# Kernel tuning notes

Measured on AMD Instinct MI355X. Metric: run time of the kernel, lower is better.

## Reference

```python
import jax, jax.numpy as jnp
import numpy as np

N = 100000   # nodes
E = 200000   # edges
L = 3        # GNN layers
D = 300      # node feature dim
H = 150      # per-direction message dim


def setup_inputs() -> dict:
    key = jax.random.key(0)
    ks = jax.random.split(key, 8)
    s = 0.05
    return {
        "x": jax.random.normal(ks[0], (N, D), jnp.float32),
        "edge_index": jax.random.randint(ks[1], (2, E), 0, N, dtype=jnp.int32),
        "Wr": jax.random.normal(ks[2], (L, 2 * D, H), jnp.float32) * s,
        "br": jax.random.normal(ks[3], (L, H), jnp.float32) * s,
        "Wc": jax.random.normal(ks[4], (L, 2 * D, H), jnp.float32) * s,
        "bc": jax.random.normal(ks[5], (L, H), jnp.float32) * s,
        "Wa": jax.random.normal(ks[6], (D, D), jnp.float32) * s,
        "ba": jax.random.normal(ks[7], (D,), jnp.float32) * s,
    }


def _gelu(z):
    return jax.nn.gelu(z, approximate=False)  # torch GELU is exact erf


def _msg_aggr(v, src, dst, W, b):
    # message at each edge: GELU(Linear(cat(x_i, x_j))), x_i = target, x_j = source
    m = _gelu(jnp.concatenate([v[dst], v[src]], axis=-1) @ W + b)  # [E, H]
    # sum-aggregate messages at target nodes
    return jax.ops.segment_sum(m, dst, num_segments=N)  # [N, H]


def reference(x, edge_index, Wr, br, Wc, bc, Wa, ba):
    src, dst = edge_index[0], edge_index[1]

    def step(v, p):
        Wr_l, br_l, Wc_l, bc_l = p
        r = _msg_aggr(v, src, dst, Wr_l, br_l)        # r2c: original direction
        c = _msg_aggr(v, dst, src, Wc_l, bc_l)        # c2r: flipped edge_index
        v = v + _gelu(jnp.concatenate([r, c], axis=-1) @ Wa + ba)
        return v, None

    out, _ = jax.lax.scan(step, x, (Wr, br, Wc, bc))
    return out
```

## Files before the change

### kernel.cpp

```cpp
#include <hip/hip_runtime.h>
#include <hip/hip_bf16.h>
#include <math.h>

#define NND 100000
#define EE  200000
#define LL  3
#define DD  300
#define HH  150

#define MPAD 100096
#define KP   320
#define NPJ  640
#define NUP  384
#define NTK  (KP / 32)

#define NB   49
#define SCN  (NB * 2048)

#define BSTRIDE 132

#define P_BR 0
#define P_BC 152
#define P_AR 304
#define P_AC 456
#define RC_R 0
#define RC_C 160

typedef __attribute__((ext_vector_type(8))) short bf16x8;
typedef __attribute__((ext_vector_type(4))) short bf16x4;
typedef __attribute__((ext_vector_type(4))) float f32x4;

__device__ __forceinline__ float gelu_exact(float z) {
    return 0.5f * z * (1.0f + erff(z * 0.7071067811865475f));
}
__device__ __forceinline__ unsigned short f2bf(float f) {
    union { float fv; unsigned u; } v; v.fv = f;
    unsigned r = v.u + 0x7fff + ((v.u >> 16) & 1);
    return (unsigned short)(r >> 16);
}
__device__ __forceinline__ float bf2f(unsigned short b) {
    union { unsigned u; float fv; } v; v.u = ((unsigned)b) << 16;
    return v.fv;
}

__global__ __launch_bounds__(256) void pack_w(
    const float* __restrict__ Wr, const float* __restrict__ Wc,
    const float* __restrict__ Wa,
    unsigned short* __restrict__ Bt, unsigned short* __restrict__ Wat)
{
    int i = blockIdx.x * 256 + threadIdx.x;
    const int btTotal = LL * NPJ * KP;
    if (i < btTotal) {
        int l = i / (NPJ * KP);
        int rem = i % (NPJ * KP);
        int n = rem / KP;
        int k = rem % KP;
        float v = 0.f;
        if (k < DD) {
            const float* W = nullptr; int krow = k, j = -1;
            if (n >= P_BR && n < P_BR + 150)      { W = Wr; krow = 300 + k; j = n - P_BR; }
            else if (n >= P_BC && n < P_BC + 150) { W = Wc; krow = 300 + k; j = n - P_BC; }
            else if (n >= P_AR && n < P_AR + 150) { W = Wr; krow = k;       j = n - P_AR; }
            else if (n >= P_AC && n < P_AC + 150) { W = Wc; krow = k;       j = n - P_AC; }
            if (j >= 0)
                v = W[(size_t)l * 600 * 150 + (size_t)krow * 150 + j];
        }
        Bt[i] = f2bf(v);
    } else {
        int i2 = i - btTotal;
        if (i2 < NUP * KP) {
            int n = i2 / KP, k = i2 % KP;
            int kk = -1;
            if (k < 150)                 kk = k;
            else if (k >= 160 && k < 310) kk = k - 10;
            float v = (n < DD && kk >= 0) ? Wa[(size_t)kk * DD + n] : 0.f;
            Wat[i2] = f2bf(v);
        }
    }
}

__global__ __launch_bounds__(256) void init_vbf(
    const float* __restrict__ x, unsigned short* __restrict__ vbf)
{
    int idx = blockIdx.x * 256 + threadIdx.x;
    int row = idx / (KP / 8);
    int gk  = (idx % (KP / 8)) * 8;
    if (row >= MPAD) return;
    unsigned short tmp[8];
    if (row < NND && gk < DD) {
        if (gk + 8 <= DD) {
            const float4* p = (const float4*)(x + (size_t)row * DD + gk);
            float4 f0 = p[0], f1 = p[1];
            tmp[0] = f2bf(f0.x); tmp[1] = f2bf(f0.y);
            tmp[2] = f2bf(f0.z); tmp[3] = f2bf(f0.w);
            tmp[4] = f2bf(f1.x); tmp[5] = f2bf(f1.y);
            tmp[6] = f2bf(f1.z); tmp[7] = f2bf(f1.w);
        } else {
            #pragma unroll
            for (int j = 0; j < 8; ++j)
                tmp[j] = (gk + j < DD) ? f2bf(x[(size_t)row * DD + gk + j]) : 0;
        }
    } else {
        #pragma unroll
        for (int j = 0; j < 8; ++j) tmp[j] = 0;
    }
    *((bf16x8*)&vbf[(size_t)row * KP + gk]) = *((bf16x8*)tmp);
}

__global__ __launch_bounds__(256) void hist_deg(
    const int* __restrict__ src, const int* __restrict__ dst,
    int* __restrict__ deg)
{
    int e = blockIdx.x * 256 + threadIdx.x;
    if (e >= EE) return;
    atomicAdd(&deg[dst[e]], 1);
    atomicAdd(&deg[SCN + src[e]], 1);
}

__global__ __launch_bounds__(256) void scanA(
    const int* __restrict__ deg, int* __restrict__ off, int* __restrict__ bsum)
{
    __shared__ int ls[256];
    const int t = threadIdx.x, row = blockIdx.y;
    const int base = blockIdx.x * 2048 + t * 8;
    const int* dg = deg + (size_t)row * SCN + base;
    int v[8];
    #pragma unroll
    for (int j = 0; j < 8; ++j) v[j] = dg[j];
    int tot = 0;
    #pragma unroll
    for (int j = 0; j < 8; ++j) tot += v[j];
    ls[t] = tot;
    __syncthreads();
    #pragma unroll
    for (int d = 1; d < 256; d <<= 1) {
        int tv = (t >= d) ? ls[t - d] : 0;
        __syncthreads();
        ls[t] += tv;
        __syncthreads();
    }
    int run = ls[t] - tot;
    int* op = off + (size_t)row * SCN + base;
    #pragma unroll
    for (int j = 0; j < 8; ++j) { op[j] = run; run += v[j]; }
    if (t == 255) bsum[row * 64 + blockIdx.x] = ls[255];
}

__global__ __launch_bounds__(256) void scanB(int* __restrict__ bsum)
{
    if (threadIdx.x < 2) {
        int row = threadIdx.x, c = 0;
        for (int i = 0; i < NB; ++i) {
            int tv = bsum[row * 64 + i];
            bsum[row * 64 + i] = c;
            c += tv;
        }
    }
}

__global__ __launch_bounds__(256) void scanC(
    int* __restrict__ off, const int* __restrict__ bsum, int* __restrict__ cur)
{
    const int t = threadIdx.x, row = blockIdx.y;
    const int base = blockIdx.x * 2048 + t * 8;
    const int add = bsum[row * 64 + blockIdx.x];
    int* op = off + (size_t)row * SCN + base;
    int* cp = cur + (size_t)row * SCN + base;
    #pragma unroll
    for (int j = 0; j < 8; ++j) {
        int v = op[j] + add;
        op[j] = v;
        cp[j] = v;
    }
}

__global__ __launch_bounds__(256) void fill_adj(
    const int* __restrict__ src, const int* __restrict__ dst,
    int* __restrict__ cur, int* __restrict__ adj)
{
    int e = blockIdx.x * 256 + threadIdx.x;
    if (e >= EE) return;
    int s = src[e], d = dst[e];
    int pd = atomicAdd(&cur[d], 1);
    adj[pd] = s;
    int ps = atomicAdd(&cur[SCN + s], 1);
    adj[EE + ps] = d;
}

__global__ __launch_bounds__(256) void aggregate(
    const int* __restrict__ off, const int* __restrict__ adj,
    const unsigned short* __restrict__ P,
    const float* __restrict__ br, const float* __restrict__ bc,
    unsigned short* __restrict__ RC)
{
    const int n    = blockIdx.x * 4 + (threadIdx.x >> 6);
    const int dir  = blockIdx.y;
    const int lane = threadIdx.x & 63;
    const int c    = lane * 4;

    if (lane < 10)
        RC[(size_t)n * KP + (dir ? 310 : 150) + lane] = 0;
    if (c >= 152) return;

    const int* offp = off + (size_t)dir * SCN;
    const int* adjp = adj + (size_t)dir * EE;
    const float* bias = dir ? bc : br;
    const unsigned short* own = P + (size_t)n * NPJ + (dir ? P_AC : P_AR);
    const int poff = dir ? P_BC : P_BR;

    const bool g0 = (c + 0) < 150, g1 = (c + 1) < 150;
    const bool g2 = (c + 2) < 150, g3 = (c + 3) < 150;

    bf16x4 ow = *((const bf16x4*)&own[c]);
    float o0 = bf2f((unsigned short)ow[0]) + (g0 ? bias[c + 0] : 0.f);
    float o1 = bf2f((unsigned short)ow[1]) + (g1 ? bias[c + 1] : 0.f);
    float o2 = bf2f((unsigned short)ow[2]) + (g2 ? bias[c + 2] : 0.f);
    float o3 = bf2f((unsigned short)ow[3]) + (g3 ? bias[c + 3] : 0.f);

    float s0 = 0.f, s1 = 0.f, s2 = 0.f, s3 = 0.f;
    int beg = offp[n], end = offp[n + 1];
    if (beg < end) {
        int a = adjp[beg];
        for (int i = beg; i < end; ++i) {
            int anext = (i + 1 < end) ? adjp[i + 1] : 0;
            const unsigned short* pp = P + (size_t)a * NPJ + poff;
            bf16x4 pv = *((const bf16x4*)&pp[c]);
            s0 += gelu_exact(o0 + bf2f((unsigned short)pv[0]));
            s1 += gelu_exact(o1 + bf2f((unsigned short)pv[1]));
            s2 += gelu_exact(o2 + bf2f((unsigned short)pv[2]));
            s3 += gelu_exact(o3 + bf2f((unsigned short)pv[3]));
            a = anext;
        }
    }
    unsigned short* outrow = RC + (size_t)n * KP + (dir ? RC_C : RC_R);
    if (c + 4 <= 150) {
        bf16x4 o;
        o[0] = (short)f2bf(s0); o[1] = (short)f2bf(s1);
        o[2] = (short)f2bf(s2); o[3] = (short)f2bf(s3);
        *((bf16x4*)&outrow[c]) = o;
    } else {
        if (g0) outrow[c + 0] = f2bf(s0);
        if (g1) outrow[c + 1] = f2bf(s1);
    }
}

#define GLOAD16(gp, lp) __builtin_amdgcn_global_load_lds( \
    (const __attribute__((address_space(1))) unsigned int*)(gp), \
    (__attribute__((address_space(3))) unsigned int*)(lp), 16, 0, 0)

template<int MODE>
__global__ __launch_bounds__(256) void gemm_breg(
    const unsigned short* __restrict__ Ab,
    const unsigned short* __restrict__ Bt,
    unsigned short* __restrict__ P,
    float* __restrict__ outv, unsigned short* __restrict__ vbf,
    const float* __restrict__ bias, int last)
{
    __shared__ char smem[64 * BSTRIDE * 4];
    unsigned short* Alds = (unsigned short*)smem;
    float* bounce = (float*)smem;

    const int tid  = threadIdx.x;
    const int lane = tid & 63;
    const int wid  = tid >> 6;

    const int gx   = gridDim.x;
    const int nwg  = gx * gridDim.y;
    const int flat = blockIdx.y * gx + blockIdx.x;
    const int q = nwg >> 3, r = nwg & 7;
    const int xcd = flat & 7, off = flat >> 3;
    const int lid = (xcd < r ? xcd * (q + 1) : r * (q + 1) + (xcd - r) * q) + off;
    const int brow = (lid / gx) * 64;
    const int bcol = (lid % gx) * 128;

    const int wn = wid * 32;

    f32x4 acc[4][2];
    #pragma unroll
    for (int i = 0; i < 4; ++i)
        #pragma unroll
        for (int j = 0; j < 2; ++j)
            #pragma unroll
            for (int rr = 0; rr < 4; ++rr) acc[i][j][rr] = 0.f;

    bf16x8 bfr[NTK][2];
    const unsigned short* Bb =
        Bt + (size_t)(bcol + wn + (lane & 15)) * KP + (lane >> 4) * 8;
    #pragma unroll
    for (int t = 0; t < NTK; ++t) {
        bfr[t][0] = *((const bf16x8*)(Bb + t * 32));
        bfr[t][1] = *((const bf16x8*)(Bb + (size_t)16 * KP + t * 32));
    }

    const int arow = tid >> 2;
    const int ac   = (tid & 3) ^ ((arow >> 1) & 3);
    const unsigned short* asrc = Ab + (size_t)(brow + arow) * KP + ac * 8;

    #pragma unroll
    for (int t = 0; t < 3; ++t)
        GLOAD16(asrc + t * 32, Alds + t * 2048 + wid * 512);

    #pragma unroll
    for (int t = 0; t < NTK; ++t) {
        unsigned short* Alc = Alds + (t & 3) * 2048;
        if (t + 2 < NTK) {
            asm volatile("s_waitcnt vmcnt(2)" ::: "memory");
        } else if (t + 1 < NTK) {
            asm volatile("s_waitcnt vmcnt(1)" ::: "memory");
        } else {
            asm volatile("s_waitcnt vmcnt(0)" ::: "memory");
        }
        __builtin_amdgcn_s_barrier();
        if (t + 3 < NTK)
            GLOAD16(asrc + (t + 3) * 32, Alds + ((t + 3) & 3) * 2048 + wid * 512);

        bf16x8 af[4];
        #pragma unroll
        for (int mi = 0; mi < 4; ++mi) {
            int row = mi * 16 + (lane & 15);
            af[mi] = *((const bf16x8*)&Alc[row * 32 + (((lane >> 4) ^ ((row >> 1) & 3)) * 8)]);
        }
        __builtin_amdgcn_s_setprio(1);
        #pragma unroll
        for (int mi = 0; mi < 4; ++mi)
            #pragma unroll
            for (int nj = 0; nj < 2; ++nj)
                acc[mi][nj] = __builtin_amdgcn_mfma_f32_16x16x32_bf16(
                    af[mi], bfr[t][nj], acc[mi][nj], 0, 0, 0);
        __builtin_amdgcn_s_setprio(0);
    }
    __syncthreads();

    #pragma unroll
    for (int mi = 0; mi < 4; ++mi)
        #pragma unroll
        for (int nj = 0; nj < 2; ++nj) {
            int lcol = wn + nj * 16 + (lane & 15);
            int rb = mi * 16 + ((lane >> 4) << 2);
            #pragma unroll
            for (int rr = 0; rr < 4; ++rr)
                bounce[(rb + rr) * BSTRIDE + lcol] = acc[mi][nj][rr];
        }
    __syncthreads();

    const int ro = tid >> 5;
    const int co = (tid & 31) * 4;
    #pragma unroll
    for (int i = 0; i < 8; ++i) {
        int lrow = ro + i * 8;
        int grow = brow + lrow;
        float4 vv = *(const float4*)&bounce[lrow * BSTRIDE + co];
        if (MODE == 0) {
            bf16x4 o;
            o[0] = (short)f2bf(vv.x); o[1] = (short)f2bf(vv.y);
            o[2] = (short)f2bf(vv.z); o[3] = (short)f2bf(vv.w);
            *((bf16x4*)&P[(size_t)grow * NPJ + bcol + co]) = o;
        } else if (grow < NND) {
            int gc = bcol + co;
            if (bcol < 256) {
                float4 bv = *(const float4*)&bias[gc];
                bf16x4 old = *(const bf16x4*)&vbf[(size_t)grow * KP + gc];
                float4 nv;
                nv.x = bf2f((unsigned short)old[0]) + gelu_exact(vv.x + bv.x);
                nv.y = bf2f((unsigned short)old[1]) + gelu_exact(vv.y + bv.y);
                nv.z = bf2f((unsigned short)old[2]) + gelu_exact(vv.z + bv.z);
                nv.w = bf2f((unsigned short)old[3]) + gelu_exact(vv.w + bv.w);
                if (last) {
                    *((float4*)&outv[(size_t)grow * DD + gc]) = nv;
                } else {
                    bf16x4 o;
                    o[0] = (short)f2bf(nv.x); o[1] = (short)f2bf(nv.y);
                    o[2] = (short)f2bf(nv.z); o[3] = (short)f2bf(nv.w);
                    *((bf16x4*)&vbf[(size_t)grow * KP + gc]) = o;
                }
            } else {
                #pragma unroll
                for (int j = 0; j < 4; ++j) {
                    int ccc = gc + j;
                    if (ccc < DD) {
                        float vj = (j == 0) ? vv.x : (j == 1) ? vv.y
                                 : (j == 2) ? vv.z : vv.w;
                        size_t vidx = (size_t)grow * KP + ccc;
                        float nv = bf2f(vbf[vidx]) + gelu_exact(vj + bias[ccc]);
                        if (last) outv[(size_t)grow * DD + ccc] = nv;
                        else      vbf[vidx] = f2bf(nv);
                    }
                }
            }
        }
    }
}

extern "C" void kernel_launch(void* const* d_in, const int* in_sizes, int n_in,
                              void* d_out, int out_size, void* d_ws, size_t ws_size,
                              hipStream_t stream) {
    const float* x  = (const float*)d_in[0];
    const int*   ei = (const int*)  d_in[1];
    const float* Wr = (const float*)d_in[2];
    const float* br = (const float*)d_in[3];
    const float* Wc = (const float*)d_in[4];
    const float* bc = (const float*)d_in[5];
    const float* Wa = (const float*)d_in[6];
    const float* ba = (const float*)d_in[7];
    float* out = (float*)d_out;

    const size_t P_elems   = (size_t)MPAD * NPJ;
    const size_t RC_elems  = (size_t)MPAD * KP;
    const size_t V_elems   = (size_t)MPAD * KP;
    const size_t Bt_elems  = (size_t)LL * NPJ * KP;
    const size_t Wat_elems = (size_t)NUP * KP;

    unsigned short* P   = (unsigned short*)d_ws;
    unsigned short* RC  = P + P_elems;
    unsigned short* vbf = RC + RC_elems;
    unsigned short* Bt  = vbf + V_elems;
    unsigned short* Wat = Bt + Bt_elems;
    int* deg  = (int*)(Wat + Wat_elems);
    int* off  = deg + 2 * SCN;
    int* curp = off + 2 * SCN;
    int* adj  = curp + 2 * SCN;
    int* bsum = adj + 2 * EE;
    const size_t need = (char*)(bsum + 128) - (char*)d_ws;
    if (ws_size < need) return;

    pack_w<<<2880, 256, 0, stream>>>(Wr, Wc, Wa, Bt, Wat);
    init_vbf<<<(int)((V_elems / 8 + 255) / 256), 256, 0, stream>>>(x, vbf);

    const int* src = ei;
    const int* dst = ei + EE;

    hipMemsetAsync(deg, 0, 2 * SCN * sizeof(int), stream);
    hist_deg<<<(EE + 255) / 256, 256, 0, stream>>>(src, dst, deg);
    scanA<<<dim3(NB, 2), 256, 0, stream>>>(deg, off, bsum);
    scanB<<<1, 256, 0, stream>>>(bsum);
    scanC<<<dim3(NB, 2), 256, 0, stream>>>(off, bsum, curp);
    fill_adj<<<(EE + 255) / 256, 256, 0, stream>>>(src, dst, curp, adj);

    dim3 gproj(NPJ / 128, MPAD / 64);
    dim3 gupd (NUP / 128, MPAD / 64);
    dim3 gagg (MPAD / 4, 2);

    for (int l = 0; l < LL; ++l) {
        gemm_breg<0><<<gproj, 256, 0, stream>>>(
            vbf, Bt + (size_t)l * NPJ * KP, P, nullptr, nullptr, nullptr, 0);
        aggregate<<<gagg, 256, 0, stream>>>(
            off, adj, P, br + (size_t)l * HH, bc + (size_t)l * HH, RC);
        gemm_breg<1><<<gupd, 256, 0, stream>>>(
            RC, Wat, nullptr, out, vbf, ba, (l == LL - 1) ? 1 : 0);
    }
}
```

Measured before the change: 1.038 ms.

## Make GEMMs persistent over row-tile chunks with cross-tile A prefetch

Result: no change. 1.025 ms (-1.2%).

```diff
diff --git a/kernel.cpp b/kernel.cpp
--- a/kernel.cpp
+++ b/kernel.cpp
@@ -9,6 +9,7 @@
 #define HH  150
 
 #define MPAD 100096
+#define MTILES 1564
 #define KP   320
 #define NPJ  640
 #define NUP  384
@@ -248,32 +249,93 @@
     (const __attribute__((address_space(1))) unsigned int*)(gp), \
     (__attribute__((address_space(3))) unsigned int*)(lp), 16, 0, 0)
 
+#define STAGE_ONE() do {                                                     \
+        GLOAD16(scur, Alds + (scnt & 3) * 2048 + wid * 512);                 \
+        scur += 32; ++scnt;                                                  \
+        if (++st_ == NTK) { st_ = 0; scur += (size_t)63 * KP; }              \
+    } while (0)
+
+#define COMPUTE_STEP(t, buf) do {                                            \
+        unsigned short* Alc_ = Alds + (buf) * 2048;                          \
+        bf16x8 af[4];                                                        \
+        _Pragma("unroll")                                                    \
+        for (int mi = 0; mi < 4; ++mi) {                                     \
+            int row_ = mi * 16 + (lane & 15);                                \
+            af[mi] = *((const bf16x8*)&Alc_[row_ * 32 +                      \
+                       (((lane >> 4) ^ ((row_ >> 1) & 3)) * 8)]);            \
+        }                                                                    \
+        __builtin_amdgcn_s_setprio(1);                                       \
+        _Pragma("unroll")                                                    \
+        for (int mi = 0; mi < 4; ++mi) {                                     \
+            acc[mi][0] = __builtin_amdgcn_mfma_f32_16x16x32_bf16(            \
+                af[mi], bfr[t][0], acc[mi][0], 0, 0, 0);                     \
+            acc[mi][1] = __builtin_amdgcn_mfma_f32_16x16x32_bf16(            \
+                af[mi], bfr[t][1], acc[mi][1], 0, 0, 0);                     \
+        }                                                                    \
+        __builtin_amdgcn_s_setprio(0);                                       \
+    } while (0)
+
 template<int MODE>
-__global__ __launch_bounds__(256) void gemm_breg(
+__global__ __launch_bounds__(256) void gemm_pers(
     const unsigned short* __restrict__ Ab,
     const unsigned short* __restrict__ Bt,
     unsigned short* __restrict__ P,
     float* __restrict__ outv, unsigned short* __restrict__ vbf,
-    const float* __restrict__ bias, int last)
-{
-    __shared__ char smem[64 * BSTRIDE * 4];
+    const float* __restrict__ bias, int last, int ncol, int chunk)
+{
+    __shared__ char smem[16384 + 64 * BSTRIDE * 4];
     unsigned short* Alds = (unsigned short*)smem;
-    float* bounce = (float*)smem;
+    float* bounce = (float*)(smem + 16384);
 
     const int tid  = threadIdx.x;
     const int lane = tid & 63;
     const int wid  = tid >> 6;
 
-    const int gx   = gridDim.x;
-    const int nwg  = gx * gridDim.y;
-    const int flat = blockIdx.y * gx + blockIdx.x;
-    const int q = nwg >> 3, r = nwg & 7;
-    const int xcd = flat & 7, off = flat >> 3;
-    const int lid = (xcd < r ? xcd * (q + 1) : r * (q + 1) + (xcd - r) * q) + off;
-    const int brow = (lid / gx) * 64;
-    const int bcol = (lid % gx) * 128;
-
-    const int wn = wid * 32;
+    const int bid  = blockIdx.x;
+    const int col  = bid % ncol;
+    const int slot = bid / ncol;
+    const int m0t  = slot * chunk;
+    int ntiles = MTILES - m0t;
+    if (ntiles > chunk) ntiles = chunk;
+    if (ntiles <= 0) return;
+    const int bcol = col * 128;
+    const int wn   = wid * 32;
+
+    bf16x8 bfr[NTK][2];
+    {
+        const unsigned short* Bb =
+            Bt + (size_t)(bcol + wn + (lane & 15)) * KP + (lane >> 4) * 8;
+        #pragma unroll
+        for (int t = 0; t < NTK; ++t) {
+            bfr[t][0] = *((const bf16x8*)(Bb + t * 32));
+            bfr[t][1] = *((const bf16x8*)(Bb + (size_t)16 * KP + t * 32));
+        }
+    }
+
+    const int ro = tid >> 5;
+    const int co = (tid & 31) * 4;
+    float4 bv = {0.f, 0.f, 0.f, 0.f};
+    float bj[4] = {0.f, 0.f, 0.f, 0.f};
+    if (MODE == 1) {
+        if (bcol < 256) {
+            bv = *((const float4*)&bias[bcol + co]);
+        } else {
+            #pragma unroll
+            for (int j = 0; j < 4; ++j) {
+                int cc = bcol + co + j;
+                if (cc < DD) bj[j] = bias[cc];
+            }
+        }
+    }
+
+    const int arow = tid >> 2;
+    const int ac   = (tid & 3) ^ ((arow >> 1) & 3);
+    const unsigned short* scur =
+        Ab + (size_t)(m0t * 64 + arow) * KP + ac * 8;
+    int st_ = 0;
+    unsigned scnt = 0;
+
+    STAGE_ONE(); STAGE_ONE(); STAGE_ONE();
 
     f32x4 acc[4][2];
     #pragma unroll
@@ -283,111 +345,98 @@
             #pragma unroll
             for (int rr = 0; rr < 4; ++rr) acc[i][j][rr] = 0.f;
 
-    bf16x8 bfr[NTK][2];
-    const unsigned short* Bb =
-        Bt + (size_t)(bcol + wn + (lane & 15)) * KP + (lane >> 4) * 8;
-    #pragma unroll
-    for (int t = 0; t < NTK; ++t) {
-        bfr[t][0] = *((const bf16x8*)(Bb + t * 32));
-        bfr[t][1] = *((const bf16x8*)(Bb + (size_t)16 * KP + t * 32));
-    }
-
-    const int arow = tid >> 2;
-    const int ac   = (tid & 3) ^ ((arow >> 1) & 3);
-    const unsigned short* asrc = Ab + (size_t)(brow + arow) * KP + ac * 8;
-
-    #pragma unroll
-    for (int t = 0; t < 3; ++t)
-        GLOAD16(asrc + t * 32, Alds + t * 2048 + wid * 512);
-
-    #pragma unroll
-    for (int t = 0; t < NTK; ++t) {
-        unsigned short* Alc = Alds + (t & 3) * 2048;
-        if (t + 2 < NTK) {
-            asm volatile("s_waitcnt vmcnt(2)" ::: "memory");
-        } else if (t + 1 < NTK) {
-            asm volatile("s_waitcnt vmcnt(1)" ::: "memory");
+    for (int g = 0; g < ntiles; ++g) {
+        const int bb = (g * 2) & 3;
+        if (g + 1 < ntiles) {
+            #pragma unroll
+            for (int t = 0; t < NTK; ++t) {
+                asm volatile("s_waitcnt vmcnt(2)" ::: "memory");
+                __builtin_amdgcn_s_barrier();
+                STAGE_ONE();
+                COMPUTE_STEP(t, (bb + t) & 3);
+            }
         } else {
-            asm volatile("s_waitcnt vmcnt(0)" ::: "memory");
-        }
-        __builtin_amdgcn_s_barrier();
-        if (t + 3 < NTK)
-            GLOAD16(asrc + (t + 3) * 32, Alds + ((t + 3) & 3) * 2048 + wid * 512);
-
-        bf16x8 af[4];
-        #pragma unroll
-        for (int mi = 0; mi < 4; ++mi) {
-            int row = mi * 16 + (lane & 15);
-            af[mi] = *((const bf16x8*)&Alc[row * 32 + (((lane >> 4) ^ ((row >> 1) & 3)) * 8)]);
-        }
-        __builtin_amdgcn_s_setprio(1);
+            #pragma unroll
+            for (int t = 0; t < NTK; ++t) {
+                if (t + 2 < NTK) {
+                    asm volatile("s_waitcnt vmcnt(2)" ::: "memory");
+                } else if (t + 1 < NTK) {
+                    asm volatile("s_waitcnt vmcnt(1)" ::: "memory");
+                } else {
+                    asm volatile("s_waitcnt vmcnt(0)" ::: "memory");
+                }
+                __builtin_amdgcn_s_barrier();
+                if (t + 3 < NTK) STAGE_ONE();
+                COMPUTE_STEP(t, (bb + t) & 3);
+            }
+        }
+
+        const int brow = (m0t + g) * 64;
         #pragma unroll
         for (int mi = 0; mi < 4; ++mi)
             #pragma unroll
-            for (int nj = 0; nj < 2; ++nj)
-                acc[mi][nj] = __builtin_amdgcn_mfma_f32_16x16x32_bf16(
-                    af[mi], bfr[t][nj], acc[mi][nj], 0, 0, 0);
-        __builtin_amdgcn_s_setprio(0);
-    }
-    __syncthreads();
-
-    #pragma unroll
-    for (int mi = 0; mi < 4; ++mi)
+            for (int nj = 0; nj < 2; ++nj) {
+                int lcol = wn + nj * 16 + (lane & 15);
+                int rb = mi * 16 + ((lane >> 4) << 2);
+                #pragma unroll
+                for (int rr = 0; rr < 4; ++rr)
+                    bounce[(rb + rr) * BSTRIDE + lcol] = acc[mi][nj][rr];
+            }
+        asm volatile("s_waitcnt lgkmcnt(0)" ::: "memory");
+        __builtin_amdgcn_sched_barrier(0);
+        __builtin_amdgcn_s_barrier();
+
         #pragma unroll
-        for (int nj = 0; nj < 2; ++nj) {
-            int lcol = wn + nj * 16 + (lane & 15);
-            int rb = mi * 16 + ((lane >> 4) << 2);
-            #pragma unroll
-            for (int rr = 0; rr < 4; ++rr)
-                bounce[(rb + rr) * BSTRIDE + lcol] = acc[mi][nj][rr];
-        }
-    __syncthreads();
-
-    const int ro = tid >> 5;
-    const int co = (tid & 31) * 4;
-    #pragma unroll
-    for (int i = 0; i < 8; ++i) {
-        int lrow = ro + i * 8;
-        int grow = brow + lrow;
-        float4 vv = *(const float4*)&bounce[lrow * BSTRIDE + co];
-        if (MODE == 0) {
-            bf16x4 o;
-            o[0] = (short)f2bf(vv.x); o[1] = (short)f2bf(vv.y);
-            o[2] = (short)f2bf(vv.z); o[3] = (short)f2bf(vv.w);
-            *((bf16x4*)&P[(size_t)grow * NPJ + bcol + co]) = o;
-        } else if (grow < NND) {
-            int gc = bcol + co;
-            if (bcol < 256) {
-                float4 bv = *(const float4*)&bias[gc];
-                bf16x4 old = *(const bf16x4*)&vbf[(size_t)grow * KP + gc];
-                float4 nv;
-                nv.x = bf2f((unsigned short)old[0]) + gelu_exact(vv.x + bv.x);
-                nv.y = bf2f((unsigned short)old[1]) + gelu_exact(vv.y + bv.y);
-                nv.z = bf2f((unsigned short)old[2]) + gelu_exact(vv.z + bv.z);
-                nv.w = bf2f((unsigned short)old[3]) + gelu_exact(vv.w + bv.w);
-                if (last) {
-                    *((float4*)&outv[(size_t)grow * DD + gc]) = nv;
+        for (int i = 0; i < 8; ++i) {
+            int lrow = ro + i * 8;
+            int grow = brow + lrow;
+            float4 vv = *(const float4*)&bounce[lrow * BSTRIDE + co];
+            if (MODE == 0) {
+                bf16x4 o;
+                o[0] = (short)f2bf(vv.x); o[1] = (short)f2bf(vv.y);
+                o[2] = (short)f2bf(vv.z); o[3] = (short)f2bf(vv.w);
+                *((bf16x4*)&P[(size_t)grow * NPJ + bcol + co]) = o;
+            } else if (grow < NND) {
+                int gc = bcol + co;
+                if (bcol < 256) {
+                    bf16x4 old = *(const bf16x4*)&vbf[(size_t)grow * KP + gc];
+                    float4 nv;
+                    nv.x = bf2f((unsigned short)old[0]) + gelu_exact(vv.x + bv.x);
+                    nv.y = bf2f((unsigned short)old[1]) + gelu_exact(vv.y + bv.y);
+                    nv.z = bf2f((unsigned short)old[2]) + gelu_exact(vv.z + bv.z);
+                    nv.w = bf2f((unsigned short)old[3]) + gelu_exact(vv.w + bv.w);
+                    if (last) {
+                        *((float4*)&outv[(size_t)grow * DD + gc]) = nv;
+                    } else {
+                        bf16x4 o;
+                        o[0] = (short)f2bf(nv.x); o[1] = (short)f2bf(nv.y);
+                        o[2] = (short)f2bf(nv.z); o[3] = (short)f2bf(nv.w);
+                        *((bf16x4*)&vbf[(size_t)grow * KP + gc]) = o;
+                    }
                 } else {
-                    bf16x4 o;
-                    o[0] = (short)f2bf(nv.x); o[1] = (short)f2bf(nv.y);
-                    o[2] = (short)f2bf(nv.z); o[3] = (short)f2bf(nv.w);
-                    *((bf16x4*)&vbf[(size_t)grow * KP + gc]) = o;
-                }
-            } else {
-                #pragma unroll
-                for (int j = 0; j < 4; ++j) {
-                    int ccc = gc + j;
-                    if (ccc < DD) {
-                        float vj = (j == 0) ? vv.x : (j == 1) ? vv.y
-                                 : (j == 2) ? vv.z : vv.w;
-                        size_t vidx = (size_t)grow * KP + ccc;
-                        float nv = bf2f(vbf[vidx]) + gelu_exact(vj + bias[ccc]);
-                        if (last) outv[(size_t)grow * DD + ccc] = nv;
-                        else      vbf[vidx] = f2bf(nv);
+                    #pragma unroll
+                    for (int j = 0; j < 4; ++j) {
+                        int ccc = gc + j;
+                        if (ccc < DD) {
+                            float vj = (j == 0) ? vv.x : (j == 1) ? vv.y
+                                     : (j == 2) ? vv.z : vv.w;
+                            size_t vidx = (size_t)grow * KP + ccc;
+                            float nv = bf2f(vbf[vidx]) + gelu_exact(vj + bj[j]);
+                            if (last) outv[(size_t)grow * DD + ccc] = nv;
+                            else      vbf[vidx] = f2bf(nv);
+                        }
                     }
                 }
             }
         }
+        __builtin_amdgcn_s_barrier();
+
+        #pragma unroll
+        for (int i = 0; i < 4; ++i)
+            #pragma unroll
+            for (int j = 0; j < 2; ++j)
+                #pragma unroll
+                for (int rr = 0; rr < 4; ++rr) acc[i][j][rr] = 0.f;
     }
 }
 
@@ -436,16 +485,20 @@
     scanC<<<dim3(NB, 2), 256, 0, stream>>>(off, bsum, curp);
     fill_adj<<<(EE + 255) / 256, 256, 0, stream>>>(src, dst, curp, adj);
 
-    dim3 gproj(NPJ / 128, MPAD / 64);
-    dim3 gupd (NUP / 128, MPAD / 64);
+    const int CHUNK_PJ = 11, SLOTS_PJ = (MTILES + CHUNK_PJ - 1) / CHUNK_PJ;
+    const int CHUNK_UP = 7,  SLOTS_UP = (MTILES + CHUNK_UP - 1) / CHUNK_UP;
+    dim3 gproj(5 * SLOTS_PJ);
+    dim3 gupd (3 * SLOTS_UP);
     dim3 gagg (MPAD / 4, 2);
 
     for (int l = 0; l < LL; ++l) {
-        gemm_breg<0><<<gproj, 256, 0, stream>>>(
-            vbf, Bt + (size_t)l * NPJ * KP, P, nullptr, nullptr, nullptr, 0);
+        gemm_pers<0><<<gproj, 256, 0, stream>>>(
+            vbf, Bt + (size_t)l * NPJ * KP, P, nullptr, nullptr, nullptr,
+            0, 5, CHUNK_PJ);
         aggregate<<<gagg, 256, 0, stream>>>(
             off, adj, P, br + (size_t)l * HH, bc + (size_t)l * HH, RC);
-        gemm_breg<1><<<gupd, 256, 0, stream>>>(
-            RC, Wat, nullptr, out, vbf, ba, (l == LL - 1) ? 1 : 0);
-    }
-}
+        gemm_pers<1><<<gupd, 256, 0, stream>>>(
+            RC, Wat, nullptr, out, vbf, ba, (l == LL - 1) ? 1 : 0,
+            3, CHUNK_UP);
+    }
+}
```

## Rewrite GEMM as per-wave register-pipelined kernel without LDS staging or block barriers

Applied to the files above, without the earlier changes.

Result: slower. 1.409 ms (+35.7%).

```diff
diff --git a/kernel.cpp b/kernel.cpp
--- a/kernel.cpp
+++ b/kernel.cpp
@@ -16,8 +16,6 @@
 
 #define NB   49
 #define SCN  (NB * 2048)
-
-#define BSTRIDE 132
 
 #define P_BR 0
 #define P_BC 152
@@ -244,21 +242,39 @@
     }
 }
 
-#define GLOAD16(gp, lp) __builtin_amdgcn_global_load_lds( \
-    (const __attribute__((address_space(1))) unsigned int*)(gp), \
-    (__attribute__((address_space(3))) unsigned int*)(lp), 16, 0, 0)
+#define LDG(dst, voff, base, OFF) \
+    asm volatile("global_load_dwordx4 %0, %1, %2 offset:" OFF \
+                 : "=v"(dst) : "v"(voff), "s"(base) : "memory")
+
+#define LOADA(S, OFF) do { \
+    LDG(ar[S][0], va0, Ab, OFF); LDG(ar[S][1], va1, Ab, OFF); } while (0)
+
+#define LOADB(S, OFF) do { \
+    LDG(brg[S][0], vb0, Bt, OFF); LDG(brg[S][1], vb1, Bt, OFF); \
+    LDG(brg[S][2], vb2, Bt, OFF); LDG(brg[S][3], vb3, Bt, OFF); } while (0)
+
+#define WAITV(N) do { \
+    asm volatile("s_waitcnt vmcnt(" #N ")" ::: "memory"); \
+    __builtin_amdgcn_sched_barrier(0); } while (0)
+
+#define MFMA8(TA, TB) do { \
+    _Pragma("unroll") \
+    for (int g_ = 0; g_ < 2; ++g_) { \
+        _Pragma("unroll") \
+        for (int nj_ = 0; nj_ < 4; ++nj_) \
+            acc[g_][nj_] = __builtin_amdgcn_mfma_f32_16x16x32_bf16( \
+                ar[TA][g_], brg[TB][nj_], acc[g_][nj_], 0, 0, 0); \
+    } } while (0)
 
 template<int MODE>
-__global__ __launch_bounds__(256) void gemm_breg(
+__global__ __launch_bounds__(256, 4) void gemm_wave(
     const unsigned short* __restrict__ Ab,
     const unsigned short* __restrict__ Bt,
     unsigned short* __restrict__ P,
     float* __restrict__ outv, unsigned short* __restrict__ vbf,
     const float* __restrict__ bias, int last)
 {
-    __shared__ char smem[64 * BSTRIDE * 4];
-    unsigned short* Alds = (unsigned short*)smem;
-    float* bounce = (float*)smem;
+    __shared__ char smem[4 * 4608];
 
     const int tid  = threadIdx.x;
     const int lane = tid & 63;
@@ -270,120 +286,88 @@
     const int q = nwg >> 3, r = nwg & 7;
     const int xcd = flat & 7, off = flat >> 3;
     const int lid = (xcd < r ? xcd * (q + 1) : r * (q + 1) + (xcd - r) * q) + off;
-    const int brow = (lid / gx) * 64;
-    const int bcol = (lid % gx) * 128;
-
-    const int wn = wid * 32;
-
-    f32x4 acc[4][2];
-    #pragma unroll
-    for (int i = 0; i < 4; ++i)
+    const int brow = (lid / gx) * 128;
+    const int bcol = (lid % gx) * 64;
+    const int wrow = brow + wid * 32;
+
+    const unsigned va0 = (unsigned)(wrow + (lane & 15)) * (KP * 2) + (lane >> 4) * 16;
+    const unsigned va1 = va0 + 16 * KP * 2;
+    const unsigned vb0 = (unsigned)(bcol + (lane & 15)) * (KP * 2) + (lane >> 4) * 16;
+    const unsigned vb1 = vb0 + 16 * KP * 2;
+    const unsigned vb2 = vb0 + 32 * KP * 2;
+    const unsigned vb3 = vb0 + 48 * KP * 2;
+
+    bf16x8 ar[4][2];
+    bf16x8 brg[2][4];
+    f32x4 acc[2][4];
+    #pragma unroll
+    for (int i = 0; i < 2; ++i)
         #pragma unroll
-        for (int j = 0; j < 2; ++j)
+        for (int j = 0; j < 4; ++j)
             #pragma unroll
             for (int rr = 0; rr < 4; ++rr) acc[i][j][rr] = 0.f;
 
-    bf16x8 bfr[NTK][2];
-    const unsigned short* Bb =
-        Bt + (size_t)(bcol + wn + (lane & 15)) * KP + (lane >> 4) * 8;
-    #pragma unroll
-    for (int t = 0; t < NTK; ++t) {
-        bfr[t][0] = *((const bf16x8*)(Bb + t * 32));
-        bfr[t][1] = *((const bf16x8*)(Bb + (size_t)16 * KP + t * 32));
-    }
-
-    const int arow = tid >> 2;
-    const int ac   = (tid & 3) ^ ((arow >> 1) & 3);
-    const unsigned short* asrc = Ab + (size_t)(brow + arow) * KP + ac * 8;
-
-    #pragma unroll
-    for (int t = 0; t < 3; ++t)
-        GLOAD16(asrc + t * 32, Alds + t * 2048 + wid * 512);
-
-    #pragma unroll
-    for (int t = 0; t < NTK; ++t) {
-        unsigned short* Alc = Alds + (t & 3) * 2048;
-        if (t + 2 < NTK) {
-            asm volatile("s_waitcnt vmcnt(2)" ::: "memory");
-        } else if (t + 1 < NTK) {
-            asm volatile("s_waitcnt vmcnt(1)" ::: "memory");
-        } else {
-            asm volatile("s_waitcnt vmcnt(0)" ::: "memory");
-        }
-        __builtin_amdgcn_s_barrier();
-        if (t + 3 < NTK)
-            GLOAD16(asrc + (t + 3) * 32, Alds + ((t + 3) & 3) * 2048 + wid * 512);
-
-        bf16x8 af[4];
+    LOADA(0, "0"); LOADA(1, "64"); LOADA(2, "128"); LOADB(0, "0");
+    LOADB(1, "64");  LOADA(3, "192"); WAITV(6); MFMA8(0, 0);
+    LOADB(0, "128"); LOADA(0, "256"); WAITV(8); MFMA8(1, 1);
+    LOADB(1, "192"); LOADA(1, "320"); WAITV(8); MFMA8(2, 0);
+    LOADB(0, "256"); LOADA(2, "384"); WAITV(8); MFMA8(3, 1);
+    LOADB(1, "320"); LOADA(3, "448"); WAITV(8); MFMA8(0, 0);
+    LOADB(0, "384"); LOADA(0, "512"); WAITV(8); MFMA8(1, 1);
+    LOADB(1, "448"); LOADA(1, "576"); WAITV(8); MFMA8(2, 0);
+    LOADB(0, "512");                  WAITV(6); MFMA8(3, 1);
+    LOADB(1, "576");                  WAITV(4); MFMA8(0, 0);
+                                      WAITV(0); MFMA8(1, 1);
+
+    if (MODE == 0) {
+        unsigned short* sb = (unsigned short*)(smem + wid * 4608);
         #pragma unroll
-        for (int mi = 0; mi < 4; ++mi) {
-            int row = mi * 16 + (lane & 15);
-            af[mi] = *((const bf16x8*)&Alc[row * 32 + (((lane >> 4) ^ ((row >> 1) & 3)) * 8)]);
-        }
-        __builtin_amdgcn_s_setprio(1);
+        for (int g = 0; g < 2; ++g)
+            #pragma unroll
+            for (int nj = 0; nj < 4; ++nj)
+                #pragma unroll
+                for (int rr = 0; rr < 4; ++rr) {
+                    int row = g * 16 + ((lane >> 4) << 2) + rr;
+                    sb[row * 72 + nj * 16 + (lane & 15)] = f2bf(acc[g][nj][rr]);
+                }
         #pragma unroll
-        for (int mi = 0; mi < 4; ++mi)
+        for (int i = 0; i < 4; ++i) {
+            int row = i * 8 + (lane >> 3);
+            bf16x8 v = *((const bf16x8*)&sb[row * 72 + (lane & 7) * 8]);
+            *((bf16x8*)&P[(size_t)(wrow + row) * NPJ + bcol + (lane & 7) * 8]) = v;
+        }
+    } else {
+        float* fb = (float*)(smem + wid * 4608);
+        const int gc = bcol + (lane & 15) * 4;
+        #pragma unroll
+        for (int h = 0; h < 2; ++h) {
             #pragma unroll
-            for (int nj = 0; nj < 2; ++nj)
-                acc[mi][nj] = __builtin_amdgcn_mfma_f32_16x16x32_bf16(
-                    af[mi], bfr[t][nj], acc[mi][nj], 0, 0, 0);
-        __builtin_amdgcn_s_setprio(0);
-    }
-    __syncthreads();
-
-    #pragma unroll
-    for (int mi = 0; mi < 4; ++mi)
-        #pragma unroll
-        for (int nj = 0; nj < 2; ++nj) {
-            int lcol = wn + nj * 16 + (lane & 15);
-            int rb = mi * 16 + ((lane >> 4) << 2);
+            for (int nj = 0; nj < 4; ++nj)
+                #pragma unroll
+                for (int rr = 0; rr < 4; ++rr) {
+                    int r16 = ((lane >> 4) << 2) + rr;
+                    fb[r16 * 68 + nj * 16 + (lane & 15)] = acc[h][nj][rr];
+                }
             #pragma unroll
-            for (int rr = 0; rr < 4; ++rr)
-                bounce[(rb + rr) * BSTRIDE + lcol] = acc[mi][nj][rr];
-        }
-    __syncthreads();
-
-    const int ro = tid >> 5;
-    const int co = (tid & 31) * 4;
-    #pragma unroll
-    for (int i = 0; i < 8; ++i) {
-        int lrow = ro + i * 8;
-        int grow = brow + lrow;
-        float4 vv = *(const float4*)&bounce[lrow * BSTRIDE + co];
-        if (MODE == 0) {
-            bf16x4 o;
-            o[0] = (short)f2bf(vv.x); o[1] = (short)f2bf(vv.y);
-            o[2] = (short)f2bf(vv.z); o[3] = (short)f2bf(vv.w);
-            *((bf16x4*)&P[(size_t)grow * NPJ + bcol + co]) = o;
-        } else if (grow < NND) {
-            int gc = bcol + co;
-            if (bcol < 256) {
-                float4 bv = *(const float4*)&bias[gc];
-                bf16x4 old = *(const bf16x4*)&vbf[(size_t)grow * KP + gc];
-                float4 nv;
-                nv.x = bf2f((unsigned short)old[0]) + gelu_exact(vv.x + bv.x);
-                nv.y = bf2f((unsigned short)old[1]) + gelu_exact(vv.y + bv.y);
-                nv.z = bf2f((unsigned short)old[2]) + gelu_exact(vv.z + bv.z);
-                nv.w = bf2f((unsigned short)old[3]) + gelu_exact(vv.w + bv.w);
-                if (last) {
-                    *((float4*)&outv[(size_t)grow * DD + gc]) = nv;
-                } else {
-                    bf16x4 o;
-                    o[0] = (short)f2bf(nv.x); o[1] = (short)f2bf(nv.y);
-                    o[2] = (short)f2bf(nv.z); o[3] = (short)f2bf(nv.w);
-                    *((bf16x4*)&vbf[(size_t)grow * KP + gc]) = o;
-                }
-            } else {
-                #pragma unroll
-                for (int j = 0; j < 4; ++j) {
-                    int ccc = gc + j;
-                    if (ccc < DD) {
-                        float vj = (j == 0) ? vv.x : (j == 1) ? vv.y
-                                 : (j == 2) ? vv.z : vv.w;
-                        size_t vidx = (size_t)grow * KP + ccc;
-                        float nv = bf2f(vbf[vidx]) + gelu_exact(vj + bias[ccc]);
-                        if (last) outv[(size_t)grow * DD + ccc] = nv;
-                        else      vbf[vidx] = f2bf(nv);
+            for (int i = 0; i < 4; ++i) {
+                int r16 = i * 4 + (lane >> 4);
+                int grow = wrow + h * 16 + r16;
+                float4 vv = *((const float4*)&fb[r16 * 68 + (lane & 15) * 4]);
+                if (grow < NND && gc + 3 < DD) {
+                    float4 bv = *((const float4*)&bias[gc]);
+                    bf16x4 old = *((const bf16x4*)&vbf[(size_t)grow * KP + gc]);
+                    float4 nv;
+                    nv.x = bf2f((unsigned short)old[0]) + gelu_exact(vv.x + bv.x);
+                    nv.y = bf2f((unsigned short)old[1]) + gelu_exact(vv.y + bv.y);
+                    nv.z = bf2f((unsigned short)old[2]) + gelu_exact(vv.z + bv.z);
+                    nv.w = bf2f((unsigned short)old[3]) + gelu_exact(vv.w + bv.w);
+                    if (last) {
+                        *((float4*)&outv[(size_t)grow * DD + gc]) = nv;
+                    } else {
+                        bf16x4 o;
+                        o[0] = (short)f2bf(nv.x); o[1] = (short)f2bf(nv.y);
+                        o[2] = (short)f2bf(nv.z); o[3] = (short)f2bf(nv.w);
+                        *((bf16x4*)&vbf[(size_t)grow * KP + gc]) = o;
                     }
                 }
             }
@@ -436,16 +420,16 @@
     scanC<<<dim3(NB, 2), 256, 0, stream>>>(off, bsum, curp);
     fill_adj<<<(EE + 255) / 256, 256, 0, stream>>>(src, dst, curp, adj);
 
-    dim3 gproj(NPJ / 128, MPAD / 64);
-    dim3 gupd (NUP / 128, MPAD / 64);
+    dim3 gproj(NPJ / 64, MPAD / 128);
+    dim3 gupd (5,        MPAD / 128);
     dim3 gagg (MPAD / 4, 2);
 
     for (int l = 0; l < LL; ++l) {
-        gemm_breg<0><<<gproj, 256, 0, stream>>>(
+        gemm_wave<0><<<gproj, 256, 0, stream>>>(
             vbf, Bt + (size_t)l * NPJ * KP, P, nullptr, nullptr, nullptr, 0);
         aggregate<<<gagg, 256, 0, stream>>>(
             off, adj, P, br + (size_t)l * HH, bc + (size_t)l * HH, RC);
-        gemm_breg<1><<<gupd, 256, 0, stream>>>(
+        gemm_wave<1><<<gupd, 256, 0, stream>>>(
             RC, Wat, nullptr, out, vbf, ba, (l == LL - 1) ? 1 : 0);
     }
 }
```

## Make GEMM A-tile staging per-wave to remove block barriers

Applied to the files above, without the earlier changes.

Measured after the change: 1.180 ms. +13.7%, slower.

```diff
diff --git a/kernel.cpp b/kernel.cpp
--- a/kernel.cpp
+++ b/kernel.cpp
@@ -16,8 +16,6 @@
 
 #define NB   49
 #define SCN  (NB * 2048)
-
-#define BSTRIDE 132
 
 #define P_BR 0
 #define P_BC 152
@@ -244,25 +242,33 @@
     }
 }
 
-#define GLOAD16(gp, lp) __builtin_amdgcn_global_load_lds( \
-    (const __attribute__((address_space(1))) unsigned int*)(gp), \
-    (__attribute__((address_space(3))) unsigned int*)(lp), 16, 0, 0)
+#define GL(psrc, ldst) __builtin_amdgcn_global_load_lds( \
+    (const __attribute__((address_space(1))) unsigned int*)(psrc), \
+    (__attribute__((address_space(3))) unsigned int*)(ldst), 16, 0, 0)
+
+#define SB0() __builtin_amdgcn_sched_barrier(0)
+
+#define STAGEP(BUF, TT) do { \
+    GL(p0 + (TT) * 32, Aw + (BUF) * 2048 + 0 * 512); \
+    GL(p1 + (TT) * 32, Aw + (BUF) * 2048 + 1 * 512); \
+    GL(p2 + (TT) * 32, Aw + (BUF) * 2048 + 2 * 512); \
+    GL(p3 + (TT) * 32, Aw + (BUF) * 2048 + 3 * 512); \
+    SB0(); } while (0)
 
 template<int MODE>
-__global__ __launch_bounds__(256) void gemm_breg(
+__global__ __launch_bounds__(256, 2) void gemm_wavp(
     const unsigned short* __restrict__ Ab,
     const unsigned short* __restrict__ Bt,
     unsigned short* __restrict__ P,
     float* __restrict__ outv, unsigned short* __restrict__ vbf,
     const float* __restrict__ bias, int last)
 {
-    __shared__ char smem[64 * BSTRIDE * 4];
-    unsigned short* Alds = (unsigned short*)smem;
-    float* bounce = (float*)smem;
+    __shared__ unsigned short smem[4 * 8192];
 
     const int tid  = threadIdx.x;
     const int lane = tid & 63;
     const int wid  = tid >> 6;
+    unsigned short* Aw = &smem[wid * 8192];
 
     const int gx   = gridDim.x;
     const int nwg  = gx * gridDim.y;
@@ -272,8 +278,34 @@
     const int lid = (xcd < r ? xcd * (q + 1) : r * (q + 1) + (xcd - r) * q) + off;
     const int brow = (lid / gx) * 64;
     const int bcol = (lid % gx) * 128;
-
-    const int wn = wid * 32;
+    const int wn   = wid * 32;
+
+    bf16x8 bfr[NTK][2];
+    {
+        const unsigned short* Bb =
+            Bt + (size_t)(bcol + wn + (lane & 15)) * KP + (lane >> 4) * 8;
+        #pragma unroll
+        for (int t = 0; t < NTK; ++t) {
+            bfr[t][0] = *((const bf16x8*)(Bb + t * 32));
+            bfr[t][1] = *((const bf16x8*)(Bb + (size_t)16 * KP + t * 32));
+        }
+    }
+    SB0();
+
+    const int r0 = (lane >> 2);
+    const unsigned short* p0; const unsigned short* p1;
+    const unsigned short* p2; const unsigned short* p3;
+    {
+        int rr0 = 0 * 16 + r0, rr1 = 1 * 16 + r0, rr2 = 2 * 16 + r0, rr3 = 3 * 16 + r0;
+        int c0 = (lane & 3) ^ ((rr0 >> 1) & 3);
+        int c1 = (lane & 3) ^ ((rr1 >> 1) & 3);
+        int c2 = (lane & 3) ^ ((rr2 >> 1) & 3);
+        int c3 = (lane & 3) ^ ((rr3 >> 1) & 3);
+        p0 = Ab + (size_t)(brow + rr0) * KP + c0 * 8;
+        p1 = Ab + (size_t)(brow + rr1) * KP + c1 * 8;
+        p2 = Ab + (size_t)(brow + rr2) * KP + c2 * 8;
+        p3 = Ab + (size_t)(brow + rr3) * KP + c3 * 8;
+    }
 
     f32x4 acc[4][2];
     #pragma unroll
@@ -283,42 +315,24 @@
             #pragma unroll
             for (int rr = 0; rr < 4; ++rr) acc[i][j][rr] = 0.f;
 
-    bf16x8 bfr[NTK][2];
-    const unsigned short* Bb =
-        Bt + (size_t)(bcol + wn + (lane & 15)) * KP + (lane >> 4) * 8;
+    STAGEP(0, 0); STAGEP(1, 1); STAGEP(2, 2);
+
     #pragma unroll
     for (int t = 0; t < NTK; ++t) {
-        bfr[t][0] = *((const bf16x8*)(Bb + t * 32));
-        bfr[t][1] = *((const bf16x8*)(Bb + (size_t)16 * KP + t * 32));
-    }
-
-    const int arow = tid >> 2;
-    const int ac   = (tid & 3) ^ ((arow >> 1) & 3);
-    const unsigned short* asrc = Ab + (size_t)(brow + arow) * KP + ac * 8;
-
-    #pragma unroll
-    for (int t = 0; t < 3; ++t)
-        GLOAD16(asrc + t * 32, Alds + t * 2048 + wid * 512);
-
-    #pragma unroll
-    for (int t = 0; t < NTK; ++t) {
-        unsigned short* Alc = Alds + (t & 3) * 2048;
-        if (t + 2 < NTK) {
-            asm volatile("s_waitcnt vmcnt(2)" ::: "memory");
-        } else if (t + 1 < NTK) {
-            asm volatile("s_waitcnt vmcnt(1)" ::: "memory");
-        } else {
-            asm volatile("s_waitcnt vmcnt(0)" ::: "memory");
-        }
-        __builtin_amdgcn_s_barrier();
-        if (t + 3 < NTK)
-            GLOAD16(asrc + (t + 3) * 32, Alds + ((t + 3) & 3) * 2048 + wid * 512);
-
+        if (t + 3 < NTK) STAGEP((t + 3) & 3, t + 3);
+        if (t <= NTK - 4)      { asm volatile("s_waitcnt vmcnt(12)" ::: "memory"); }
+        else if (t == NTK - 3) { asm volatile("s_waitcnt vmcnt(8)"  ::: "memory"); }
+        else if (t == NTK - 2) { asm volatile("s_waitcnt vmcnt(4)"  ::: "memory"); }
+        else                   { asm volatile("s_waitcnt vmcnt(0)"  ::: "memory"); }
+        SB0();
+
+        const unsigned short* Alc = Aw + (t & 3) * 2048;
         bf16x8 af[4];
         #pragma unroll
         for (int mi = 0; mi < 4; ++mi) {
             int row = mi * 16 + (lane & 15);
-            af[mi] = *((const bf16x8*)&Alc[row * 32 + (((lane >> 4) ^ ((row >> 1) & 3)) * 8)]);
+            af[mi] = *((const bf16x8*)&Alc[row * 32 +
+                       (((lane >> 4) ^ ((row >> 1) & 3)) * 8)]);
         }
         __builtin_amdgcn_s_setprio(1);
         #pragma unroll
@@ -329,61 +343,71 @@
                     af[mi], bfr[t][nj], acc[mi][nj], 0, 0, 0);
         __builtin_amdgcn_s_setprio(0);
     }
-    __syncthreads();
-
-    #pragma unroll
-    for (int mi = 0; mi < 4; ++mi)
-        #pragma unroll
-        for (int nj = 0; nj < 2; ++nj) {
-            int lcol = wn + nj * 16 + (lane & 15);
-            int rb = mi * 16 + ((lane >> 4) << 2);
+
+    if (MODE == 0) {
+        #pragma unroll
+        for (int mi = 0; mi < 4; ++mi)
             #pragma unroll
-            for (int rr = 0; rr < 4; ++rr)
-                bounce[(rb + rr) * BSTRIDE + lcol] = acc[mi][nj][rr];
-        }
-    __syncthreads();
-
-    const int ro = tid >> 5;
-    const int co = (tid & 31) * 4;
-    #pragma unroll
-    for (int i = 0; i < 8; ++i) {
-        int lrow = ro + i * 8;
-        int grow = brow + lrow;
-        float4 vv = *(const float4*)&bounce[lrow * BSTRIDE + co];
-        if (MODE == 0) {
-            bf16x4 o;
-            o[0] = (short)f2bf(vv.x); o[1] = (short)f2bf(vv.y);
-            o[2] = (short)f2bf(vv.z); o[3] = (short)f2bf(vv.w);
-            *((bf16x4*)&P[(size_t)grow * NPJ + bcol + co]) = o;
-        } else if (grow < NND) {
-            int gc = bcol + co;
-            if (bcol < 256) {
-                float4 bv = *(const float4*)&bias[gc];
-                bf16x4 old = *(const bf16x4*)&vbf[(size_t)grow * KP + gc];
-                float4 nv;
-                nv.x = bf2f((unsigned short)old[0]) + gelu_exact(vv.x + bv.x);
-                nv.y = bf2f((unsigned short)old[1]) + gelu_exact(vv.y + bv.y);
-                nv.z = bf2f((unsigned short)old[2]) + gelu_exact(vv.z + bv.z);
-                nv.w = bf2f((unsigned short)old[3]) + gelu_exact(vv.w + bv.w);
-                if (last) {
-                    *((float4*)&outv[(size_t)grow * DD + gc]) = nv;
+            for (int nj = 0; nj < 2; ++nj)
+                #pragma unroll
+                for (int rr = 0; rr < 4; ++rr) {
+                    int row = mi * 16 + ((lane >> 4) << 2) + rr;
+                    int col = nj * 16 + (lane & 15);
+                    Aw[row * 40 + col] = f2bf(acc[mi][nj][rr]);
+                }
+        #pragma unroll
+        for (int i = 0; i < 4; ++i) {
+            int row = i * 16 + (lane >> 2);
+            bf16x8 v = *((const bf16x8*)&Aw[row * 40 + (lane & 3) * 8]);
+            *((bf16x8*)&P[(size_t)(brow + row) * NPJ + bcol + wn + (lane & 3) * 8]) = v;
+        }
+    } else {
+        float* fb = (float*)Aw;
+        #pragma unroll
+        for (int mi = 0; mi < 4; ++mi)
+            #pragma unroll
+            for (int nj = 0; nj < 2; ++nj)
+                #pragma unroll
+                for (int rr = 0; rr < 4; ++rr) {
+                    int row = mi * 16 + ((lane >> 4) << 2) + rr;
+                    int col = nj * 16 + (lane & 15);
+                    fb[row * 36 + col] = acc[mi][nj][rr];
+                }
+        const int gc = bcol + wn + (lane & 7) * 4;
+        #pragma unroll
+        for (int i = 0; i < 8; ++i) {
+            int row = i * 8 + (lane >> 3);
+            int grow = brow + row;
+            float4 vv = *((const float4*)&fb[row * 36 + (lane & 7) * 4]);
+            if (grow < NND) {
+                if (gc + 4 <= DD) {
+                    float4 bv = *((const float4*)&bias[gc]);
+                    bf16x4 old = *((const bf16x4*)&vbf[(size_t)grow * KP + gc]);
+                    float4 nv;
+                    nv.x = bf2f((unsigned short)old[0]) + gelu_exact(vv.x + bv.x);
+                    nv.y = bf2f((unsigned short)old[1]) + gelu_exact(vv.y + bv.y);
+                    nv.z = bf2f((unsigned short)old[2]) + gelu_exact(vv.z + bv.z);
+                    nv.w = bf2f((unsigned short)old[3]) + gelu_exact(vv.w + bv.w);
+                    if (last) {
+                        *((float4*)&outv[(size_t)grow * DD + gc]) = nv;
+                    } else {
+                        bf16x4 o;
+                        o[0] = (short)f2bf(nv.x); o[1] = (short)f2bf(nv.y);
+                        o[2] = (short)f2bf(nv.z); o[3] = (short)f2bf(nv.w);
+                        *((bf16x4*)&vbf[(size_t)grow * KP + gc]) = o;
+                    }
                 } else {
-                    bf16x4 o;
-                    o[0] = (short)f2bf(nv.x); o[1] = (short)f2bf(nv.y);
-                    o[2] = (short)f2bf(nv.z); o[3] = (short)f2bf(nv.w);
-                    *((bf16x4*)&vbf[(size_t)grow * KP + gc]) = o;
-                }
-            } else {
-                #pragma unroll
-                for (int j = 0; j < 4; ++j) {
-                    int ccc = gc + j;
-                    if (ccc < DD) {
-                        float vj = (j == 0) ? vv.x : (j == 1) ? vv.y
-                                 : (j == 2) ? vv.z : vv.w;
-                        size_t vidx = (size_t)grow * KP + ccc;
-                        float nv = bf2f(vbf[vidx]) + gelu_exact(vj + bias[ccc]);
-                        if (last) outv[(size_t)grow * DD + ccc] = nv;
-                        else      vbf[vidx] = f2bf(nv);
+                    #pragma unroll
+                    for (int j = 0; j < 4; ++j) {
+                        int ccc = gc + j;
+                        if (ccc < DD) {
+                            float vj = (j == 0) ? vv.x : (j == 1) ? vv.y
+                                     : (j == 2) ? vv.z : vv.w;
+                            size_t vidx = (size_t)grow * KP + ccc;
+                            float nv = bf2f(vbf[vidx]) + gelu_exact(vj + bias[ccc]);
+                            if (last) outv[(size_t)grow * DD + ccc] = nv;
+                            else      vbf[vidx] = f2bf(nv);
+                        }
                     }
                 }
             }
@@ -441,11 +465,11 @@
     dim3 gagg (MPAD / 4, 2);
 
     for (int l = 0; l < LL; ++l) {
-        gemm_breg<0><<<gproj, 256, 0, stream>>>(
+        gemm_wavp<0><<<gproj, 256, 0, stream>>>(
             vbf, Bt + (size_t)l * NPJ * KP, P, nullptr, nullptr, nullptr, 0);
         aggregate<<<gagg, 256, 0, stream>>>(
             off, adj, P, br + (size_t)l * HH, bc + (size_t)l * HH, RC);
-        gemm_breg<1><<<gupd, 256, 0, stream>>>(
+        gemm_wavp<1><<<gupd, 256, 0, stream>>>(
             RC, Wat, nullptr, out, vbf, ba, (l == LL - 1) ? 1 : 0);
     }
 }
```
